# Optimization experiments

Measured on AMD Instinct MI355X. Metric: run time of the kernel, lower is better.

## Reference

```python
import jax, jax.numpy as jnp
import numpy as np
from jax import lax

T, Nn, K, IN, H1, H2, G, P, HEADS = 64, 2048, 32, 256, 128, 128, 256, 60, 3


def setup_inputs() -> dict:
    key = jax.random.key(0)
    ks = jax.random.split(key, 20)
    s = 0.05  # weight scale to keep activations sane
    return {
        'h': jax.random.normal(ks[0], (T, Nn, IN), jnp.float32),
        'neigh': jax.random.randint(ks[1], (Nn, K), 0, Nn),
        'Npop': jnp.ones((1,), jnp.float32) * 1e6,
        'I': jax.random.uniform(ks[2], (T,), jnp.float32) * 1e4,
        'R': jax.random.uniform(ks[3], (T,), jnp.float32) * 1e4,
        'S': jax.random.uniform(ks[4], (T,), jnp.float32) * 9e5,
        'It': jax.random.uniform(ks[5], (T,), jnp.float32),
        'Rt': jax.random.uniform(ks[6], (T,), jnp.float32),
        'fc1': jax.random.normal(ks[7], (HEADS, IN, H1), jnp.float32) * s,
        'fc2': jax.random.normal(ks[8], (HEADS * H1, H2), jnp.float32) * s,
        'gru_Wih': jax.random.normal(ks[9], (3 * G, H2), jnp.float32) * s,
        'gru_Whh': jax.random.normal(ks[10], (3 * G, G), jnp.float32) * s,
        'gru_bih': jax.random.normal(ks[11], (3 * G,), jnp.float32) * s,
        'gru_bhh': jax.random.normal(ks[12], (3 * G,), jnp.float32) * s,
        'res1_W': jax.random.normal(ks[13], (2 * P, G + 2), jnp.float32) * s,
        'res1_b': jax.random.normal(ks[14], (2 * P,), jnp.float32) * s,
        'res2_W': jax.random.normal(ks[15], (2, G + 2), jnp.float32) * s,
        'res2_b': jax.random.normal(ks[16], (2,), jnp.float32) * s,
        'hx0': jax.random.normal(ks[17], (G,), jnp.float32),
    }


def _input_attention(iz, neigh):
    # cosine^4 edge scores, unnormalized weighted sum of neighbor feats
    src = iz[neigh]                                  # [N,K,d]
    dot = jnp.einsum('nkd,nd->nk', src, iz)
    nsrc = jnp.sqrt(jnp.einsum('nkd,nkd->nk', src, src))
    ndst = jnp.sqrt(jnp.sum(iz * iz, axis=-1))[:, None]
    e = (dot / nsrc / ndst) ** 4                     # [N,K]
    return jnp.einsum('nk,nkd->nd', e, src)


def _gat_head(x, W, neigh):
    # dot-product edge attention + per-node softmax + weighted reduce
    z = x @ W                                        # [N,H]
    src = z[neigh]                                   # [N,K,H]
    e = jnp.einsum('nkd,nd->nk', src, z)             # [N,K]
    a = jax.nn.softmax(e, axis=1)
    return jnp.einsum('nk,nkd->nd', a, src)


def _gru_cell(x, hx, Wih, Whh, bih, bhh):
    gi = Wih @ x + bih                               # [3G]
    gh = Whh @ hx + bhh
    ir, iz, inn = jnp.split(gi, 3)
    hr, hz, hn = jnp.split(gh, 3)
    r = jax.nn.sigmoid(ir + hr)
    zg = jax.nn.sigmoid(iz + hz)
    n = jnp.tanh(inn + r * hn)
    return (1.0 - zg) * n + zg * hx


def reference(h, neigh, Npop, I, R, S, It, Rt, fc1, fc2, gru_Wih, gru_Whh,
              gru_bih, gru_bhh, res1_W, res1_b, res2_W, res2_b, hx0):
    Np = Npop[0]

    def step(hx, xs):
        h_t, I_t, R_t, S_t, It_t, Rt_t = xs
        ih = _input_attention(h_t, neigh)                       # [N,in]
        heads = jax.vmap(lambda W: _gat_head(ih, W, neigh))(fc1)  # [3,N,H1]
        c = jax.nn.relu(jnp.transpose(heads, (1, 0, 2)).reshape(Nn, HEADS * H1))
        c = _gat_head(c, fc2, neigh)                            # [N,H2]
        pooled = jnp.max(jax.nn.relu(c), axis=0)                # [H2]
        hx = _gru_cell(pooled, hx, gru_Wih, gru_Whh, gru_bih, gru_bhh)
        nhx = jnp.concatenate([hx, It_t[None], Rt_t[None]])     # [G+2]
        pred = res1_W @ nhx + res1_b                            # [2P]
        ab = res2_W @ nhx + res2_b
        a_s = jax.nn.sigmoid(ab[0])
        b_s = jax.nn.sigmoid(ab[1])
        new_I = pred[0::2]
        new_R = pred[1::2]

        def sir(st, _):
            lI, lR, lS = st
            dI = a_s * lI * (lS / Np) - b_s * lI
            dR = b_s * lI
            nI = lI + lax.stop_gradient(dI)
            nR = lR + lax.stop_gradient(dR)
            nS = Np - nI - nR
            return (nI, nR, nS), (dI, dR)

        _, (pI, pR) = lax.scan(sir, (I_t, R_t, S_t), None, length=P)
        return hx, (new_I, new_R, pI, pR)

    _, (new_I, new_R, phy_I, phy_R) = lax.scan(step, hx0, (h, I, R, S, It, Rt))
    return (new_I, new_R, phy_I.reshape(-1), phy_R.reshape(-1))
```

## Files before the change

### kernel.cpp

```cpp
#include <hip/hip_runtime.h>
#include <hip/hip_bf16.h>
#include <math.h>

#define T_STEPS 64
#define NN      2048
#define KN      32
#define IND     256
#define H1D     128
#define C1D     384
#define H2D     128
#define GD      256
#define PD      60
#define GRU_NB  8

#define BITREV5_INIT {0,16,8,24,4,20,12,28,2,18,10,26,6,22,14,30, \
                      1,17,9,25,5,21,13,29,3,19,11,27,7,23,15,31}

__device__ __forceinline__ float bcast_lane(float v, int lane_imm) {
    return __uint_as_float(__builtin_amdgcn_readlane(__float_as_uint(v), lane_imm));
}

__device__ __forceinline__ float xpose_reduce16(float part[16], int lane) {
#pragma unroll
    for (int i = 0; i < 8; ++i) {
        float send = (lane & 2) ? part[i] : part[i + 8];
        float keep = (lane & 2) ? part[i + 8] : part[i];
        part[i] = keep + __shfl_xor(send, 2);
    }
#pragma unroll
    for (int i = 0; i < 4; ++i) {
        float send = (lane & 4) ? part[i] : part[i + 4];
        float keep = (lane & 4) ? part[i + 4] : part[i];
        part[i] = keep + __shfl_xor(send, 4);
    }
#pragma unroll
    for (int i = 0; i < 2; ++i) {
        float send = (lane & 8) ? part[i] : part[i + 2];
        float keep = (lane & 8) ? part[i + 2] : part[i];
        part[i] = keep + __shfl_xor(send, 8);
    }
    {
        float send = (lane & 16) ? part[0] : part[1];
        float keep = (lane & 16) ? part[1] : part[0];
        part[0] = keep + __shfl_xor(send, 16);
    }
    return part[0] + __shfl_xor(part[0], 32);
}

__global__ __launch_bounds__(256) void norms_kernel(const float* __restrict__ h,
                                                    float* __restrict__ norms,
                                                    int t_base) {
    int gw   = (int)((blockIdx.x * blockDim.x + threadIdx.x) >> 6);
    int lane = threadIdx.x & 63;
    int n    = gw & (NN - 1);
    int tloc = gw >> 11;
    const float* row = h + ((size_t)(t_base + tloc) * NN + n) * IND;
    float s = 0.f;
#pragma unroll
    for (int q = 0; q < 4; ++q) { float v = row[lane + 64 * q]; s += v * v; }
#pragma unroll
    for (int off = 32; off > 0; off >>= 1) s += __shfl_xor(s, off);
    if (lane == 0) norms[(size_t)tloc * NN + n] = sqrtf(s);
}

__global__ __launch_bounds__(256, 4) void input_attn_kernel(const float* __restrict__ h,
                                                            const int* __restrict__ neigh,
                                                            const float* __restrict__ norms,
                                                            float* __restrict__ ih,
                                                            int t_base) {
    const int BR[32] = BITREV5_INIT;
    __shared__ float hd_s[2][2][32];
    int wave    = threadIdx.x >> 6;
    int nodeloc = wave >> 1;
    int half    = wave & 1;
    int lane    = threadIdx.x & 63;
    int gw   = (int)((blockIdx.x << 1) | nodeloc);
    int n    = gw & (NN - 1);
    int tloc = gw >> 11;
    const float* hT  = h + (size_t)(t_base + tloc) * NN * IND;
    const float* nrm = norms + (size_t)tloc * NN;

    const float* dst = hT + (size_t)n * IND + half * 128;
    float d0 = dst[lane], d1 = dst[lane + 64];

    int   jreg = neigh[n * KN + (lane & 31)];
    float nj   = nrm[jreg];
    float ndst = nrm[n];

    float r0[32], r1[32], comb[16];
#pragma unroll
    for (int i = 0; i < 16; ++i) {
        int sja = __builtin_amdgcn_readlane(jreg, BR[i]);
        int sjb = __builtin_amdgcn_readlane(jreg, BR[i + 16]);
        const float* sa = hT + (size_t)sja * IND + half * 128;
        const float* sb = hT + (size_t)sjb * IND + half * 128;
        r0[i]      = sa[lane]; r1[i]      = sa[lane + 64];
        r0[i + 16] = sb[lane]; r1[i + 16] = sb[lane + 64];
        float pa = r0[i] * d0 + r1[i] * d1;
        float pb = r0[i + 16] * d0 + r1[i + 16] * d1;
        float send = (lane & 1) ? pa : pb;
        float keep = (lane & 1) ? pb : pa;
        comb[i] = keep + __shfl_xor(send, 1);
    }
#pragma unroll
    for (int i = 0; i < 32; ++i) asm volatile("" : "+v"(r0[i]), "+v"(r1[i]));
    float hdot = xpose_reduce16(comb, lane);
    if (lane < 32) hd_s[nodeloc][half][lane] = hdot;
    __syncthreads();
    float dot = hdot + hd_s[nodeloc][half ^ 1][lane & 31];

    float r  = dot / (nj * ndst);
    float r2 = r * r;
    float e  = r2 * r2;

    float a0 = 0.f, a1 = 0.f;
#pragma unroll
    for (int i = 0; i < 32; ++i) {
        float ek = bcast_lane(e, BR[i]);
        a0 += ek * r0[i];
        a1 += ek * r1[i];
    }
    float* orow = ih + (size_t)gw * IND + half * 128;
    orow[lane]      = a0;
    orow[lane + 64] = a1;
}

__global__ __launch_bounds__(256) void matmul_f32(const float* __restrict__ A,
                                                  const float* __restrict__ B,
                                                  float* __restrict__ C,
                                                  int M, int N, int K) {
    __shared__ float As[16][65];
    __shared__ float Bs[16][68];
    int tid  = threadIdx.x;
    int row0 = blockIdx.y * 64;
    int col0 = blockIdx.x * 64;
    int tr = tid >> 4, tc = tid & 15;
    float acc[4][4] = {};
    int la_m = tid >> 2;
    int la_k = (tid & 3) * 4;
    int lb_k = tid >> 4;
    int lb_n = (tid & 15) * 4;
    for (int k0 = 0; k0 < K; k0 += 16) {
        float4 av = *(const float4*)(A + (size_t)(row0 + la_m) * K + k0 + la_k);
        float4 bv = *(const float4*)(B + (size_t)(k0 + lb_k) * N + col0 + lb_n);
        __syncthreads();
        As[la_k + 0][la_m] = av.x; As[la_k + 1][la_m] = av.y;
        As[la_k + 2][la_m] = av.z; As[la_k + 3][la_m] = av.w;
        *(float4*)&Bs[lb_k][lb_n] = bv;
        __syncthreads();
#pragma unroll
        for (int kk = 0; kk < 16; ++kk) {
            float a[4], b[4];
#pragma unroll
            for (int r = 0; r < 4; ++r) a[r] = As[kk][tr * 4 + r];
#pragma unroll
            for (int c = 0; c < 4; ++c) b[c] = Bs[kk][tc * 4 + c];
#pragma unroll
            for (int r = 0; r < 4; ++r)
#pragma unroll
                for (int c = 0; c < 4; ++c) acc[r][c] += a[r] * b[c];
        }
    }
#pragma unroll
    for (int r = 0; r < 4; ++r) {
        float4 v = { acc[r][0], acc[r][1], acc[r][2], acc[r][3] };
        *(float4*)(C + (size_t)(row0 + tr * 4 + r) * N + col0 + tc * 4) = v;
    }
}

__global__ __launch_bounds__(192, 4) void gat_heads_kernel(const float* __restrict__ z1,
                                                           const int* __restrict__ neigh,
                                                           float* __restrict__ c) {
    const int BR[32] = BITREV5_INIT;
    int n    = blockIdx.x & (NN - 1);
    const float* ztbl = z1 + (size_t)(blockIdx.x >> 11) * NN * C1D;
    int head = threadIdx.x >> 6;
    int lane = threadIdx.x & 63;

    const float* dst = ztbl + (size_t)n * C1D + head * H1D;
    float d0 = dst[lane], d1 = dst[lane + 64];
    int jreg = neigh[n * KN + (lane & 31)];

    float r0[32], r1[32], comb[16];
#pragma unroll
    for (int i = 0; i < 16; ++i) {
        int sja = __builtin_amdgcn_readlane(jreg, BR[i]);
        int sjb = __builtin_amdgcn_readlane(jreg, BR[i + 16]);
        const float* sa = ztbl + (size_t)sja * C1D + head * H1D;
        const float* sb = ztbl + (size_t)sjb * C1D + head * H1D;
        r0[i]      = sa[lane]; r1[i]      = sa[lane + 64];
        r0[i + 16] = sb[lane]; r1[i + 16] = sb[lane + 64];
        float pa = r0[i] * d0 + r1[i] * d1;
        float pb = r0[i + 16] * d0 + r1[i + 16] * d1;
        float send = (lane & 1) ? pa : pb;
        float keep = (lane & 1) ? pb : pa;
        comb[i] = keep + __shfl_xor(send, 1);
    }
#pragma unroll
    for (int i = 0; i < 32; ++i) asm volatile("" : "+v"(r0[i]), "+v"(r1[i]));
    float dot = xpose_reduce16(comb, lane);

    float m = dot;
#pragma unroll
    for (int off = 16; off > 0; off >>= 1) m = fmaxf(m, __shfl_xor(m, off));
    float p = __expf(dot - m);
    float s = p;
#pragma unroll
    for (int off = 16; off > 0; off >>= 1) s += __shfl_xor(s, off);
    p /= s;

    float a0 = 0.f, a1 = 0.f;
#pragma unroll
    for (int i = 0; i < 32; ++i) {
        float pk = bcast_lane(p, BR[i]);
        a0 += pk * r0[i];
        a1 += pk * r1[i];
    }
    size_t base = (size_t)blockIdx.x * C1D + (size_t)head * H1D;
    c[base + lane]      = fmaxf(a0, 0.f);
    c[base + lane + 64] = fmaxf(a1, 0.f);
}

__global__ __launch_bounds__(256, 4) void gat_final_kernel(const float* __restrict__ z2,
                                                           const int* __restrict__ neigh,
                                                           float* __restrict__ c2) {
    const int BR[32] = BITREV5_INIT;
    int gw   = (int)((blockIdx.x << 2) | (threadIdx.x >> 6));
    int n    = gw & (NN - 1);
    const float* ztbl = z2 + (size_t)(gw >> 11) * NN * H2D;
    int lane = threadIdx.x & 63;

    const float* dst = ztbl + (size_t)n * H2D;
    float d0 = dst[lane], d1 = dst[lane + 64];
    int jreg = neigh[n * KN + (lane & 31)];

    float r0[32], r1[32], comb[16];
#pragma unroll
    for (int i = 0; i < 16; ++i) {
        int sja = __builtin_amdgcn_readlane(jreg, BR[i]);
        int sjb = __builtin_amdgcn_readlane(jreg, BR[i + 16]);
        const float* sa = ztbl + (size_t)sja * H2D;
        const float* sb = ztbl + (size_t)sjb * H2D;
        r0[i]      = sa[lane]; r1[i]      = sa[lane + 64];
        r0[i + 16] = sb[lane]; r1[i + 16] = sb[lane + 64];
        float pa = r0[i] * d0 + r1[i] * d1;
        float pb = r0[i + 16] * d0 + r1[i + 16] * d1;
        float send = (lane & 1) ? pa : pb;
        float keep = (lane & 1) ? pb : pa;
        comb[i] = keep + __shfl_xor(send, 1);
    }
#pragma unroll
    for (int i = 0; i < 32; ++i) asm volatile("" : "+v"(r0[i]), "+v"(r1[i]));
    float dot = xpose_reduce16(comb, lane);

    float m = dot;
#pragma unroll
    for (int off = 16; off > 0; off >>= 1) m = fmaxf(m, __shfl_xor(m, off));
    float p = __expf(dot - m);
    float s = p;
#pragma unroll
    for (int off = 16; off > 0; off >>= 1) s += __shfl_xor(s, off);
    p /= s;

    float a0 = 0.f, a1 = 0.f;
#pragma unroll
    for (int i = 0; i < 32; ++i) {
        float pk = bcast_lane(p, BR[i]);
        a0 += pk * r0[i];
        a1 += pk * r1[i];
    }
    c2[(size_t)gw * H2D + lane]      = fmaxf(a0, 0.f);
    c2[(size_t)gw * H2D + lane + 64] = fmaxf(a1, 0.f);
}

__global__ __launch_bounds__(128) void pool_part_kernel(const float* __restrict__ c2,
                                                        float* __restrict__ ppart) {
    int j = threadIdx.x;
    int tloc  = blockIdx.x >> 4;
    int slice = blockIdx.x & 15;
    const float* base = c2 + ((size_t)tloc * NN + slice * 128) * H2D;
    float mx = 0.f;
    for (int q = 0; q < 128; ++q) mx = fmaxf(mx, base[(size_t)q * H2D + j]);
    ppart[(size_t)blockIdx.x * H2D + j] = mx;
}
__global__ __launch_bounds__(128) void pool_reduce_kernel(const float* __restrict__ ppart,
                                                          float* __restrict__ pooled,
                                                          int t_base) {
    int j = threadIdx.x;
    const float* base = ppart + (size_t)blockIdx.x * 16 * H2D;
    float mx = 0.f;
#pragma unroll
    for (int q = 0; q < 16; ++q) mx = fmaxf(mx, base[(size_t)q * H2D + j]);
    pooled[(t_base + blockIdx.x) * H2D + j] = mx;
}

__global__ void prep_W1(const float* __restrict__ fc1, float* __restrict__ W1,
                        unsigned int* __restrict__ cnt) {
    int i = blockIdx.x * 256 + threadIdx.x;
    if (i < 256 * 384) {
        int d = i / 384, cf = i % 384;
        int hd = cf >> 7, j = cf & 127;
        W1[i] = fc1[(size_t)hd * 256 * 128 + (size_t)d * 128 + j];
    }
    if (i < T_STEPS) cnt[i] = 0u;
}

__global__ __launch_bounds__(256) void gi_all_kernel(const float* __restrict__ Wih,
                                                     const float* __restrict__ bih,
                                                     const float* __restrict__ pooled,
                                                     float* __restrict__ gi_all) {
    __shared__ float p_s[H2D];
    int t  = blockIdx.x / 3;
    int ob = (blockIdx.x % 3) * 256;
    if (threadIdx.x < H2D) p_s[threadIdx.x] = pooled[t * H2D + threadIdx.x];
    __syncthreads();
    int o = ob + threadIdx.x;
    float acc = bih[o];
    const float* wr = Wih + (size_t)o * H2D;
#pragma unroll 4
    for (int d = 0; d < H2D; ++d) acc += wr[d] * p_s[d];
    gi_all[t * 768 + o] = acc;
}

__global__ __launch_bounds__(768) void gru_reg_kernel(const float* __restrict__ Whh,
                                                      const float* __restrict__ bhh,
                                                      const float* __restrict__ gi_all,
                                                      const float* __restrict__ hx0,
                                                      float* hx_all,
                                                      unsigned int* cnt) {
    __shared__ float4 hx_pad[72];
    __shared__ __align__(16) float hx_lin[GD];
    __shared__ float gh_s[96];
    int b   = blockIdx.x;
    int tid = threadIdx.x;
    int row_local = tid >> 3;
    int sub       = tid & 7;
    int chunk     = row_local >> 5;
    int r_in      = row_local & 31;
    int grow      = chunk * GD + b * 32 + r_in;

    float4 wreg[8];
    const float4* wrow = (const float4*)(Whh + (size_t)grow * GD + sub * 32);
#pragma unroll
    for (int i = 0; i < 8; ++i) wreg[i] = wrow[i];
    float bias = (sub == 0) ? bhh[grow] : 0.f;

    for (int t = 0; t < T_STEPS; ++t) {
        if (t > 0) {
            if (tid == 0) {
                while (__hip_atomic_load(&cnt[t - 1], __ATOMIC_ACQUIRE,
                                         __HIP_MEMORY_SCOPE_AGENT) < GRU_NB)
                    __builtin_amdgcn_s_sleep(1);
            }
            __syncthreads();
        }
        const float* hsrc = (t == 0) ? hx0 : (hx_all + (size_t)(t - 1) * GD);
        if (tid < 64) {
            float4 v;
            v.x = __hip_atomic_load(hsrc + tid * 4 + 0, __ATOMIC_RELAXED, __HIP_MEMORY_SCOPE_AGENT);
            v.y = __hip_atomic_load(hsrc + tid * 4 + 1, __ATOMIC_RELAXED, __HIP_MEMORY_SCOPE_AGENT);
            v.z = __hip_atomic_load(hsrc + tid * 4 + 2, __ATOMIC_RELAXED, __HIP_MEMORY_SCOPE_AGENT);
            v.w = __hip_atomic_load(hsrc + tid * 4 + 3, __ATOMIC_RELAXED, __HIP_MEMORY_SCOPE_AGENT);
            hx_pad[(tid >> 3) * 9 + (tid & 7)] = v;
            ((float4*)hx_lin)[tid] = v;
        }
        __syncthreads();

        float acc = 0.f;
#pragma unroll
        for (int i = 0; i < 8; ++i) {
            float4 hv = hx_pad[sub * 9 + i];
            float4 wv = wreg[i];
            acc += wv.x * hv.x + wv.y * hv.y + wv.z * hv.z + wv.w * hv.w;
        }
        acc += __shfl_xor(acc, 1);
        acc += __shfl_xor(acc, 2);
        acc += __shfl_xor(acc, 4);
        if (sub == 0) gh_s[row_local] = acc + bias;
        __syncthreads();

        if (tid < 32) {
            int u = b * 32 + tid;
            float gi_r = gi_all[t * 768 + u];
            float gi_z = gi_all[t * 768 + 256 + u];
            float gi_n = gi_all[t * 768 + 512 + u];
            float r  = 1.f / (1.f + expf(-(gi_r + gh_s[tid])));
            float zg = 1.f / (1.f + expf(-(gi_z + gh_s[32 + tid])));
            float nn = tanhf(gi_n + r * gh_s[64 + tid]);
            float hnew = (1.f - zg) * nn + zg * hx_lin[u];
            __hip_atomic_store(&hx_all[(size_t)t * GD + u], hnew,
                               __ATOMIC_RELAXED, __HIP_MEMORY_SCOPE_AGENT);
            __threadfence();
        }
        __syncthreads();
        if (tid == 0)
            __hip_atomic_fetch_add(&cnt[t], 1u, __ATOMIC_RELEASE,
                                   __HIP_MEMORY_SCOPE_AGENT);
    }
}

__global__ __launch_bounds__(128) void res_sir_kernel(const float* __restrict__ hx_all,
                                                      const float* __restrict__ It,
                                                      const float* __restrict__ Rt,
                                                      const float* __restrict__ r1W,
                                                      const float* __restrict__ r1b,
                                                      const float* __restrict__ r2W,
                                                      const float* __restrict__ r2b,
                                                      const float* __restrict__ I,
                                                      const float* __restrict__ R,
                                                      const float* __restrict__ S,
                                                      const float* __restrict__ Npop,
                                                      float* __restrict__ out) {
    __shared__ float nhx[258];
    __shared__ float ab_s[2];
    int t = blockIdx.x, tid = threadIdx.x;
    for (int i = tid; i < GD; i += 128) nhx[i] = hx_all[t * GD + i];
    if (tid == 0) { nhx[256] = It[t]; nhx[257] = Rt[t]; }
    __syncthreads();
    if (tid < 120) {
        float acc = r1b[tid];
        const float* wr = r1W + tid * 258;
        for (int d = 0; d < 258; ++d) acc += wr[d] * nhx[d];
        int idx = t * 60 + (tid >> 1);
        if (tid & 1) out[3840 + idx] = acc;
        else         out[idx] = acc;
    }
    if (tid == 120 || tid == 121) {
        int q = tid - 120;
        float acc = r2b[q];
        const float* wr = r2W + q * 258;
        for (int d = 0; d < 258; ++d) acc += wr[d] * nhx[d];
        ab_s[q] = acc;
    }
    __syncthreads();
    if (tid == 0) {
        float a_s = 1.f / (1.f + expf(-ab_s[0]));
        float b_s = 1.f / (1.f + expf(-ab_s[1]));
        float Np = Npop[0];
        float lI = I[t], lR = R[t], lS = S[t];
        for (int p = 0; p < PD; ++p) {
            float dI = a_s * lI * (lS / Np) - b_s * lI;
            float dR = b_s * lI;
            lI += dI;
            lR += dR;
            lS = Np - lI - lR;
            out[7680  + t * 60 + p] = dI;
            out[11520 + t * 60 + p] = dR;
        }
    }
}

extern "C" void kernel_launch(void* const* d_in, const int* in_sizes, int n_in,
                              void* d_out, int out_size, void* d_ws, size_t ws_size,
                              hipStream_t stream) {
    const float* h    = (const float*)d_in[0];
    const int*   ng   = (const int*)  d_in[1];
    const float* Npop = (const float*)d_in[2];
    const float* I_   = (const float*)d_in[3];
    const float* R_   = (const float*)d_in[4];
    const float* S_   = (const float*)d_in[5];
    const float* It   = (const float*)d_in[6];
    const float* Rt   = (const float*)d_in[7];
    const float* fc1  = (const float*)d_in[8];
    const float* fc2  = (const float*)d_in[9];
    const float* gWih = (const float*)d_in[10];
    const float* gWhh = (const float*)d_in[11];
    const float* gbih = (const float*)d_in[12];
    const float* gbhh = (const float*)d_in[13];
    const float* r1W  = (const float*)d_in[14];
    const float* r1b  = (const float*)d_in[15];
    const float* r2W  = (const float*)d_in[16];
    const float* r2b  = (const float*)d_in[17];
    const float* hx0  = (const float*)d_in[18];
    float* out = (float*)d_out;

    char* w = (char*)d_ws;
    float* pooled = (float*)w; w += (size_t)T_STEPS * H2D * 4;
    float* hx_all = (float*)w; w += (size_t)T_STEPS * GD * 4;
    float* W1     = (float*)w; w += (size_t)256 * 384 * 4;
    float* gi_all = (float*)w; w += (size_t)T_STEPS * 768 * 4;
    float* ppart  = (float*)w; w += (size_t)T_STEPS * 16 * H2D * 4;
    unsigned int* cnt = (unsigned int*)w; w += 256;
    size_t fixed = (size_t)(w - (char*)d_ws);

    int Tc = 16;
    while (Tc > 1) {
        size_t need = fixed + (size_t)Tc * (8192 + 2ull * 2048 * 384 * 4);
        if (need <= ws_size) break;
        Tc >>= 1;
    }
    float* norms = (float*)w; w += (size_t)Tc * NN * 4;
    float* bufA  = (float*)w; w += (size_t)Tc * NN * C1D * 4;
    float* bufB  = (float*)w;

    prep_W1<<<(256 * 384 + 255) / 256, 256, 0, stream>>>(fc1, W1, cnt);

    for (int t0 = 0; t0 < T_STEPS; t0 += Tc) {
        int M = Tc * NN;
        norms_kernel      <<<Tc * NN / 4, 256, 0, stream>>>(h, norms, t0);
        input_attn_kernel <<<Tc * NN / 2, 256, 0, stream>>>(h, ng, norms, bufA, t0);
        matmul_f32<<<dim3(384 / 64, M / 64), 256, 0, stream>>>(bufA, W1, bufB, M, 384, 256);
        gat_heads_kernel  <<<Tc * NN, 192, 0, stream>>>(bufB, ng, bufA);
        matmul_f32<<<dim3(128 / 64, M / 64), 256, 0, stream>>>(bufA, fc2, bufB, M, 128, 384);
        gat_final_kernel  <<<Tc * NN / 4, 256, 0, stream>>>(bufB, ng, bufA);
        pool_part_kernel  <<<Tc * 16, 128, 0, stream>>>(bufA, ppart);
        pool_reduce_kernel<<<Tc, 128, 0, stream>>>(ppart, pooled, t0);
    }

    gi_all_kernel<<<T_STEPS * 3, 256, 0, stream>>>(gWih, gbih, pooled, gi_all);
    gru_reg_kernel<<<GRU_NB, 768, 0, stream>>>(gWhh, gbhh, gi_all, hx0, hx_all, cnt);
    res_sir_kernel<<<T_STEPS, 128, 0, stream>>>(hx_all, It, Rt, r1W, r1b, r2W, r2b,
                                                I_, R_, S_, Npop, out);
}
```

Before: 1.602 ms.

## Replace FP32 SIMT matmuls with split-bf16 (3-term) MFMA GEMMs

The two dense projections (256->384 and 384->128) move from a scalar FP32 tiled matmul to an MFMA 16x16x32 bf16 kernel. Producer kernels now write each activation as a hi/lo bf16 pair, and a prep kernel pre-transposes and splits both weight matrices, so three MFMAs per tile approximate FP32 accuracy. The new GEMM reads its operands straight from global memory with no LDS staging, and the workspace layout is changed so buffers alias. The norms kernel is also vectorised to float4, and a threadfence is dropped in the GRU kernel.

```diff
diff --git a/kernel.cpp b/kernel.cpp
--- a/kernel.cpp
+++ b/kernel.cpp
@@ -13,11 +13,20 @@
 #define PD      60
 #define GRU_NB  8
 
+typedef __attribute__((ext_vector_type(8))) short bf16x8v;
+typedef __attribute__((ext_vector_type(4))) float f32x4v;
+
 #define BITREV5_INIT {0,16,8,24,4,20,12,28,2,18,10,26,6,22,14,30, \
                       1,17,9,25,5,21,13,29,3,19,11,27,7,23,15,31}
 
 __device__ __forceinline__ float bcast_lane(float v, int lane_imm) {
     return __uint_as_float(__builtin_amdgcn_readlane(__float_as_uint(v), lane_imm));
+}
+
+__device__ __forceinline__ void bf16_split(float v, __hip_bfloat16* hi, __hip_bfloat16* lo) {
+    __hip_bfloat16 h = __float2bfloat16(v);
+    *hi = h;
+    *lo = __float2bfloat16(v - __bfloat162float(h));
 }
 
 __device__ __forceinline__ float xpose_reduce16(float part[16], int lane) {
@@ -54,10 +63,9 @@
     int lane = threadIdx.x & 63;
     int n    = gw & (NN - 1);
     int tloc = gw >> 11;
-    const float* row = h + ((size_t)(t_base + tloc) * NN + n) * IND;
-    float s = 0.f;
-#pragma unroll
-    for (int q = 0; q < 4; ++q) { float v = row[lane + 64 * q]; s += v * v; }
+    const float4* row = (const float4*)(h + ((size_t)(t_base + tloc) * NN + n) * IND);
+    float4 v = row[lane];
+    float s = v.x * v.x + v.y * v.y + v.z * v.z + v.w * v.w;
 #pragma unroll
     for (int off = 32; off > 0; off >>= 1) s += __shfl_xor(s, off);
     if (lane == 0) norms[(size_t)tloc * NN + n] = sqrtf(s);
@@ -66,7 +74,8 @@
 __global__ __launch_bounds__(256, 4) void input_attn_kernel(const float* __restrict__ h,
                                                             const int* __restrict__ neigh,
                                                             const float* __restrict__ norms,
-                                                            float* __restrict__ ih,
+                                                            __hip_bfloat16* __restrict__ ihHi,
+                                                            __hip_bfloat16* __restrict__ ihLo,
                                                             int t_base) {
     const int BR[32] = BITREV5_INIT;
     __shared__ float hd_s[2][2][32];
@@ -120,57 +129,55 @@
         a0 += ek * r0[i];
         a1 += ek * r1[i];
     }
-    float* orow = ih + (size_t)gw * IND + half * 128;
-    orow[lane]      = a0;
-    orow[lane + 64] = a1;
-}
-
-__global__ __launch_bounds__(256) void matmul_f32(const float* __restrict__ A,
-                                                  const float* __restrict__ B,
-                                                  float* __restrict__ C,
-                                                  int M, int N, int K) {
-    __shared__ float As[16][65];
-    __shared__ float Bs[16][68];
-    int tid  = threadIdx.x;
-    int row0 = blockIdx.y * 64;
-    int col0 = blockIdx.x * 64;
-    int tr = tid >> 4, tc = tid & 15;
-    float acc[4][4] = {};
-    int la_m = tid >> 2;
-    int la_k = (tid & 3) * 4;
-    int lb_k = tid >> 4;
-    int lb_n = (tid & 15) * 4;
-    for (int k0 = 0; k0 < K; k0 += 16) {
-        float4 av = *(const float4*)(A + (size_t)(row0 + la_m) * K + k0 + la_k);
-        float4 bv = *(const float4*)(B + (size_t)(k0 + lb_k) * N + col0 + lb_n);
-        __syncthreads();
-        As[la_k + 0][la_m] = av.x; As[la_k + 1][la_m] = av.y;
-        As[la_k + 2][la_m] = av.z; As[la_k + 3][la_m] = av.w;
-        *(float4*)&Bs[lb_k][lb_n] = bv;
-        __syncthreads();
-#pragma unroll
-        for (int kk = 0; kk < 16; ++kk) {
-            float a[4], b[4];
-#pragma unroll
-            for (int r = 0; r < 4; ++r) a[r] = As[kk][tr * 4 + r];
-#pragma unroll
-            for (int c = 0; c < 4; ++c) b[c] = Bs[kk][tc * 4 + c];
-#pragma unroll
-            for (int r = 0; r < 4; ++r)
-#pragma unroll
-                for (int c = 0; c < 4; ++c) acc[r][c] += a[r] * b[c];
+    size_t base = (size_t)gw * IND + half * 128;
+    __hip_bfloat16 hi, lo;
+    bf16_split(a0, &hi, &lo);
+    ihHi[base + lane] = hi;       ihLo[base + lane] = lo;
+    bf16_split(a1, &hi, &lo);
+    ihHi[base + lane + 64] = hi;  ihLo[base + lane + 64] = lo;
+}
+
+__global__ __launch_bounds__(256) void gemm_bf16x3(const __hip_bfloat16* __restrict__ Ahi,
+                                                   const __hip_bfloat16* __restrict__ Alo,
+                                                   const __hip_bfloat16* __restrict__ BThi,
+                                                   const __hip_bfloat16* __restrict__ BTlo,
+                                                   float* __restrict__ C,
+                                                   int M, int N, int K) {
+    int lane = threadIdx.x & 63;
+    int w    = threadIdx.x >> 6;
+    int m0   = blockIdx.y * 64 + w * 16;
+    int n0   = blockIdx.x * 64;
+    int r    = lane & 15;
+    int g    = lane >> 4;
+
+    const __hip_bfloat16* arow_hi = Ahi + (size_t)(m0 + r) * K + g * 8;
+    const __hip_bfloat16* arow_lo = Alo + (size_t)(m0 + r) * K + g * 8;
+
+    f32x4v acc[4] = {};
+    for (int k0 = 0; k0 < K; k0 += 32) {
+        bf16x8v ah = *(const bf16x8v*)(arow_hi + k0);
+        bf16x8v al = *(const bf16x8v*)(arow_lo + k0);
+#pragma unroll
+        for (int nt = 0; nt < 4; ++nt) {
+            size_t boff = (size_t)(n0 + nt * 16 + r) * K + g * 8 + k0;
+            bf16x8v bh = *(const bf16x8v*)(BThi + boff);
+            bf16x8v bl = *(const bf16x8v*)(BTlo + boff);
+            acc[nt] = __builtin_amdgcn_mfma_f32_16x16x32_bf16(ah, bh, acc[nt], 0, 0, 0);
+            acc[nt] = __builtin_amdgcn_mfma_f32_16x16x32_bf16(ah, bl, acc[nt], 0, 0, 0);
+            acc[nt] = __builtin_amdgcn_mfma_f32_16x16x32_bf16(al, bh, acc[nt], 0, 0, 0);
         }
     }
 #pragma unroll
-    for (int r = 0; r < 4; ++r) {
-        float4 v = { acc[r][0], acc[r][1], acc[r][2], acc[r][3] };
-        *(float4*)(C + (size_t)(row0 + tr * 4 + r) * N + col0 + tc * 4) = v;
-    }
+    for (int nt = 0; nt < 4; ++nt)
+#pragma unroll
+        for (int q = 0; q < 4; ++q)
+            C[(size_t)(m0 + g * 4 + q) * N + n0 + nt * 16 + r] = acc[nt][q];
 }
 
 __global__ __launch_bounds__(192, 4) void gat_heads_kernel(const float* __restrict__ z1,
                                                            const int* __restrict__ neigh,
-                                                           float* __restrict__ c) {
+                                                           __hip_bfloat16* __restrict__ cHi,
+                                                           __hip_bfloat16* __restrict__ cLo) {
     const int BR[32] = BITREV5_INIT;
     int n    = blockIdx.x & (NN - 1);
     const float* ztbl = z1 + (size_t)(blockIdx.x >> 11) * NN * C1D;
@@ -217,8 +224,11 @@
         a1 += pk * r1[i];
     }
     size_t base = (size_t)blockIdx.x * C1D + (size_t)head * H1D;
-    c[base + lane]      = fmaxf(a0, 0.f);
-    c[base + lane + 64] = fmaxf(a1, 0.f);
+    __hip_bfloat16 hi, lo;
+    bf16_split(fmaxf(a0, 0.f), &hi, &lo);
+    cHi[base + lane] = hi;       cLo[base + lane] = lo;
+    bf16_split(fmaxf(a1, 0.f), &hi, &lo);
+    cHi[base + lane + 64] = hi;  cLo[base + lane + 64] = lo;
 }
 
 __global__ __launch_bounds__(256, 4) void gat_final_kernel(const float* __restrict__ z2,
@@ -294,13 +304,25 @@
     pooled[(t_base + blockIdx.x) * H2D + j] = mx;
 }
 
-__global__ void prep_W1(const float* __restrict__ fc1, float* __restrict__ W1,
-                        unsigned int* __restrict__ cnt) {
+__global__ void prep_kernel(const float* __restrict__ fc1, const float* __restrict__ fc2,
+                            __hip_bfloat16* __restrict__ W1Thi, __hip_bfloat16* __restrict__ W1Tlo,
+                            __hip_bfloat16* __restrict__ f2Thi, __hip_bfloat16* __restrict__ f2Tlo,
+                            unsigned int* __restrict__ cnt) {
     int i = blockIdx.x * 256 + threadIdx.x;
-    if (i < 256 * 384) {
-        int d = i / 384, cf = i % 384;
+    if (i < 384 * 256) {
+        int cf = i / 256, d = i % 256;
         int hd = cf >> 7, j = cf & 127;
-        W1[i] = fc1[(size_t)hd * 256 * 128 + (size_t)d * 128 + j];
+        float v = fc1[(size_t)hd * 256 * 128 + (size_t)d * 128 + j];
+        __hip_bfloat16 hi, lo;
+        bf16_split(v, &hi, &lo);
+        W1Thi[i] = hi; W1Tlo[i] = lo;
+    }
+    if (i < 128 * 384) {
+        int n = i / 384, k = i % 384;
+        float v = fc2[(size_t)k * 128 + n];
+        __hip_bfloat16 hi, lo;
+        bf16_split(v, &hi, &lo);
+        f2Thi[i] = hi; f2Tlo[i] = lo;
     }
     if (i < T_STEPS) cnt[i] = 0u;
 }
@@ -390,7 +412,6 @@
             float hnew = (1.f - zg) * nn + zg * hx_lin[u];
             __hip_atomic_store(&hx_all[(size_t)t * GD + u], hnew,
                                __ATOMIC_RELAXED, __HIP_MEMORY_SCOPE_AGENT);
-            __threadfence();
         }
         __syncthreads();
         if (tid == 0)
@@ -477,33 +498,46 @@
     char* w = (char*)d_ws;
     float* pooled = (float*)w; w += (size_t)T_STEPS * H2D * 4;
     float* hx_all = (float*)w; w += (size_t)T_STEPS * GD * 4;
-    float* W1     = (float*)w; w += (size_t)256 * 384 * 4;
     float* gi_all = (float*)w; w += (size_t)T_STEPS * 768 * 4;
     float* ppart  = (float*)w; w += (size_t)T_STEPS * 16 * H2D * 4;
+    __hip_bfloat16* W1Thi = (__hip_bfloat16*)w; w += (size_t)384 * 256 * 2;
+    __hip_bfloat16* W1Tlo = (__hip_bfloat16*)w; w += (size_t)384 * 256 * 2;
+    __hip_bfloat16* f2Thi = (__hip_bfloat16*)w; w += (size_t)128 * 384 * 2;
+    __hip_bfloat16* f2Tlo = (__hip_bfloat16*)w; w += (size_t)128 * 384 * 2;
     unsigned int* cnt = (unsigned int*)w; w += 256;
     size_t fixed = (size_t)(w - (char*)d_ws);
 
+    const size_t perTc = 8192 + 2097152 + 3145728 + 3145728;
     int Tc = 16;
     while (Tc > 1) {
-        size_t need = fixed + (size_t)Tc * (8192 + 2ull * 2048 * 384 * 4);
-        if (need <= ws_size) break;
+        if (fixed + (size_t)Tc * perTc <= ws_size) break;
         Tc >>= 1;
     }
-    float* norms = (float*)w; w += (size_t)Tc * NN * 4;
-    float* bufA  = (float*)w; w += (size_t)Tc * NN * C1D * 4;
-    float* bufB  = (float*)w;
-
-    prep_W1<<<(256 * 384 + 255) / 256, 256, 0, stream>>>(fc1, W1, cnt);
+    float* norms = (float*)w;             w += (size_t)Tc * NN * 4;
+    char*  pairA = w;                     w += (size_t)Tc * NN * 256 * 2 * 2;
+    float* z1    = (float*)w;             w += (size_t)Tc * NN * C1D * 4;
+    __hip_bfloat16* cHi = (__hip_bfloat16*)w; w += (size_t)Tc * NN * C1D * 2;
+    __hip_bfloat16* cLo = (__hip_bfloat16*)w;
+
+    __hip_bfloat16* ihHi = (__hip_bfloat16*)pairA;
+    __hip_bfloat16* ihLo = ihHi + (size_t)Tc * NN * 256;
+    float* z2 = (float*)pairA;
+    float* c2 = z2 + (size_t)Tc * NN * H2D;
+
+    prep_kernel<<<(384 * 256 + 255) / 256, 256, 0, stream>>>(fc1, fc2, W1Thi, W1Tlo,
+                                                             f2Thi, f2Tlo, cnt);
 
     for (int t0 = 0; t0 < T_STEPS; t0 += Tc) {
         int M = Tc * NN;
         norms_kernel      <<<Tc * NN / 4, 256, 0, stream>>>(h, norms, t0);
-        input_attn_kernel <<<Tc * NN / 2, 256, 0, stream>>>(h, ng, norms, bufA, t0);
-        matmul_f32<<<dim3(384 / 64, M / 64), 256, 0, stream>>>(bufA, W1, bufB, M, 384, 256);
-        gat_heads_kernel  <<<Tc * NN, 192, 0, stream>>>(bufB, ng, bufA);
-        matmul_f32<<<dim3(128 / 64, M / 64), 256, 0, stream>>>(bufA, fc2, bufB, M, 128, 384);
-        gat_final_kernel  <<<Tc * NN / 4, 256, 0, stream>>>(bufB, ng, bufA);
-        pool_part_kernel  <<<Tc * 16, 128, 0, stream>>>(bufA, ppart);
+        input_attn_kernel <<<Tc * NN / 2, 256, 0, stream>>>(h, ng, norms, ihHi, ihLo, t0);
+        gemm_bf16x3<<<dim3(384 / 64, M / 64), 256, 0, stream>>>(ihHi, ihLo, W1Thi, W1Tlo,
+                                                                z1, M, 384, 256);
+        gat_heads_kernel  <<<Tc * NN, 192, 0, stream>>>(z1, ng, cHi, cLo);
+        gemm_bf16x3<<<dim3(128 / 64, M / 64), 256, 0, stream>>>(cHi, cLo, f2Thi, f2Tlo,
+                                                                z2, M, 128, 384);
+        gat_final_kernel  <<<Tc * NN / 4, 256, 0, stream>>>(z2, ng, c2);
+        pool_part_kernel  <<<Tc * 16, 128, 0, stream>>>(c2, ppart);
         pool_reduce_kernel<<<Tc, 128, 0, stream>>>(ppart, pooled, t0);
     }
 
```

Result: slower. 1.695 ms (+5.8%).
